# Kernel tuning notes

Measured on AMD Instinct MI355X. Metric: run time of the kernel, lower is better.

## Reference

```python
import jax, jax.numpy as jnp
import numpy as np

GS = 14           # group_size = (14, 14); N must equal GS*GS
NUM_HEADS = 4
DIM = 128
POS_DIM = (DIM // 4) // 4  # 8
EPS = 1e-5


def _ln(x, g, b):
    mu = x.mean(-1, keepdims=True)
    var = ((x - mu) ** 2).mean(-1, keepdims=True)
    return (x - mu) * jax.lax.rsqrt(var + EPS) * g + b


def setup_inputs() -> dict:
    key = jax.random.key(0)
    ks = jax.random.split(key, 20)
    B, N, C = 1024, GS * GS, DIM
    s = lambda fan: 1.0 / np.sqrt(fan)
    inp = {
        "x": jax.random.normal(ks[0], (B, N, C), jnp.float32),
        # linear weights stored as [in, out] (torch W.T)
        "wq": jax.random.normal(ks[1], (C, C), jnp.float32) * s(C),
        "wkv": jax.random.normal(ks[2], (C, 2 * C), jnp.float32) * s(C),
        "wproj": jax.random.normal(ks[3], (C, C), jnp.float32) * s(C),
        "bproj": jnp.zeros((C,), jnp.float32),
        "pp_w": jax.random.normal(ks[4], (2, POS_DIM), jnp.float32) * s(2),
        "pp_b": jnp.zeros((POS_DIM,), jnp.float32),
        "ln1_g": jnp.ones((POS_DIM,), jnp.float32),
        "ln1_b": jnp.zeros((POS_DIM,), jnp.float32),
        "l1_w": jax.random.normal(ks[5], (POS_DIM, POS_DIM), jnp.float32) * s(POS_DIM),
        "l1_b": jnp.zeros((POS_DIM,), jnp.float32),
        "ln2_g": jnp.ones((POS_DIM,), jnp.float32),
        "ln2_b": jnp.zeros((POS_DIM,), jnp.float32),
        "l2_w": jax.random.normal(ks[6], (POS_DIM, POS_DIM), jnp.float32) * s(POS_DIM),
        "l2_b": jnp.zeros((POS_DIM,), jnp.float32),
        "ln3_g": jnp.ones((POS_DIM,), jnp.float32),
        "ln3_b": jnp.zeros((POS_DIM,), jnp.float32),
        "l3_w": jax.random.normal(ks[7], (POS_DIM, NUM_HEADS), jnp.float32) * s(POS_DIM),
        "l3_b": jnp.zeros((NUM_HEADS,), jnp.float32),
    }
    return inp


def _rel_pos_index():
    # relative_position_index for square window (len(group_size)==2 branch)
    ch = jnp.arange(GS)
    coords = jnp.stack(jnp.meshgrid(ch, ch, indexing="ij"))        # [2, GS, GS]
    cf = coords.reshape(2, -1)                                       # [2, N]
    rel = cf[:, :, None] - cf[:, None, :]                            # [2, N, N]
    rel = rel.transpose(1, 2, 0)                                     # [N, N, 2]
    rel = rel + jnp.array([GS - 1, GS - 1])
    idx = rel[..., 0] * (2 * GS - 1) + rel[..., 1]                   # [N, N]
    return idx


def _biases():
    p = jnp.arange(1 - GS, GS)
    b = jnp.stack(jnp.meshgrid(p, p, indexing="ij"))                 # [2, 2GS-1, 2GS-1]
    return b.reshape(2, -1).T.astype(jnp.float32)                    # [(2GS-1)^2, 2]


def reference(x, wq, wkv, wproj, bproj, pp_w, pp_b,
              ln1_g, ln1_b, l1_w, l1_b,
              ln2_g, ln2_b, l2_w, l2_b,
              ln3_g, ln3_b, l3_w, l3_b):
    B, N, C = x.shape
    H = NUM_HEADS
    hd = C // H
    scale = hd ** -0.5

    q = (x @ wq).reshape(B, N, H, hd).transpose(0, 2, 1, 3)          # [B,H,N,hd]
    kv = (x @ wkv).reshape(B, N, 2, H, hd)
    k = kv[:, :, 0].transpose(0, 2, 1, 3)                            # [B,H,N,hd]
    v = kv[:, :, 1].transpose(0, 2, 1, 3)

    attn = jnp.einsum("bhqd,bhkd->bhqk", q, k) * scale               # [B,H,N,N]

    # dynamic position bias: tiny MLP over relative coords, residual=False path
    pos = _biases() @ pp_w + pp_b                                    # [M, pos_dim]
    pos = jax.nn.relu(_ln(pos, ln1_g, ln1_b)) @ l1_w + l1_b
    pos = jax.nn.relu(_ln(pos, ln2_g, ln2_b)) @ l2_w + l2_b
    pos = jax.nn.relu(_ln(pos, ln3_g, ln3_b)) @ l3_w + l3_b          # [M, H]

    rpb = pos[_rel_pos_index()]                                      # [N,N,H] gather
    attn = attn + rpb.transpose(2, 0, 1)[None]                       # [B,H,N,N]

    attn = jax.nn.softmax(attn, axis=-1)
    out = jnp.einsum("bhqk,bhkd->bhqd", attn, v)                     # [B,H,N,hd]
    out = out.transpose(0, 2, 1, 3).reshape(B, N, C)
    return out @ wproj + bproj
```

## Files before the change

kernel.cpp:

```cpp
#include <hip/hip_runtime.h>

typedef __attribute__((ext_vector_type(8))) __bf16 bf16x8;
typedef __attribute__((ext_vector_type(4))) __bf16 bf16x4;
typedef __attribute__((ext_vector_type(4))) float f32x4;
typedef __attribute__((ext_vector_type(4))) short s16x4;

#define MFMA32(a,b,c) __builtin_amdgcn_mfma_f32_16x16x32_bf16(a, b, c, 0, 0, 0)

static __device__ inline f32x4 MFMAX16(s16x4 a, s16x4 b, f32x4 c) {
#if __has_builtin(__builtin_amdgcn_mfma_f32_16x16x16bf16_1k)
  return __builtin_amdgcn_mfma_f32_16x16x16bf16_1k(a, b, c, 0, 0, 0);
#else
  f32x4 d;
  asm("v_mfma_f32_16x16x16_bf16 %0, %1, %2, %3" : "=v"(d) : "v"(a), "v"(b), "v"(c));
  return d;
#endif
}

#define KS 36
#define VS 212
#define NW 4

__device__ inline bf16x8 load_a_f32(const float* p) {
  const float4* q = (const float4*)p;
  float4 u = q[0], v = q[1];
  bf16x8 r;
  r[0] = (__bf16)u.x; r[1] = (__bf16)u.y; r[2] = (__bf16)u.z; r[3] = (__bf16)u.w;
  r[4] = (__bf16)v.x; r[5] = (__bf16)v.y; r[6] = (__bf16)v.z; r[7] = (__bf16)v.w;
  return r;
}

__device__ inline void lnrelu8(float* v, const float* g, const float* bta) {
  float mu = 0.f;
#pragma unroll
  for (int i = 0; i < 8; i++) mu += v[i];
  mu *= 0.125f;
  float var = 0.f;
#pragma unroll
  for (int i = 0; i < 8; i++) { float d = v[i] - mu; var += d * d; }
  var *= 0.125f;
  float inv = rsqrtf(var + 1e-5f);
#pragma unroll
  for (int i = 0; i < 8; i++) v[i] = fmaxf((v[i] - mu) * inv * g[i] + bta[i], 0.f);
}

__global__ void k_prep(const float* __restrict__ wq, const float* __restrict__ wkv,
                       const float* __restrict__ wproj,
                       const float* __restrict__ pp_w, const float* __restrict__ pp_b,
                       const float* ln1_g, const float* ln1_b, const float* l1_w, const float* l1_b,
                       const float* ln2_g, const float* ln2_b, const float* l2_w, const float* l2_b,
                       const float* ln3_g, const float* ln3_b, const float* l3_w, const float* l3_b,
                       __bf16* __restrict__ wF, __bf16* __restrict__ wpT,
                       __bf16* __restrict__ biasT) {
  __shared__ float pos_s[4 * 729];
  int blk = blockIdx.x, tid = threadIdx.x;
  if (blk < 88) {
    int t = blk * 256 + tid;
    if (t < 6144) {
      int lane = t & 63, frag = t >> 6;
      int kc = frag & 3, nt = (frag >> 2) & 1, tt = (frag >> 3) % 3, h = frag / 24;
      int col = lane & 15, quad = lane >> 4;
      int o = h * 32 + nt * 16 + col;
      int ibase = kc * 32 + quad * 8;
      bf16x8 vv;
#pragma unroll
      for (int j = 0; j < 8; j++) {
        int in = ibase + j;
        float w = (tt == 0) ? wq[in * 128 + o]
                : (tt == 1) ? wkv[in * 256 + o]
                            : wkv[in * 256 + 128 + o];
        vv[j] = (__bf16)w;
      }
      *(bf16x8*)&wF[(size_t)t * 8] = vv;
    } else if (t < 6144 + 16384) {
      int t2 = t - 6144;
      int o = t2 >> 7, i = t2 & 127;
      wpT[t2] = (__bf16)wproj[i * 128 + o];
    }
    return;
  }
  for (int m = tid; m < 729; m += 256) {
    float dr = (float)(m / 27) - 13.f, dc = (float)(m % 27) - 13.f;
    float a[8], bv[8];
#pragma unroll
    for (int j = 0; j < 8; j++) a[j] = dr * pp_w[j] + dc * pp_w[8 + j] + pp_b[j];
    lnrelu8(a, ln1_g, ln1_b);
#pragma unroll
    for (int o = 0; o < 8; o++) {
      float s = l1_b[o];
#pragma unroll
      for (int j = 0; j < 8; j++) s += a[j] * l1_w[j * 8 + o];
      bv[o] = s;
    }
    lnrelu8(bv, ln2_g, ln2_b);
#pragma unroll
    for (int o = 0; o < 8; o++) {
      float s = l2_b[o];
#pragma unroll
      for (int j = 0; j < 8; j++) s += bv[j] * l2_w[j * 8 + o];
      a[o] = s;
    }
    lnrelu8(a, ln3_g, ln3_b);
#pragma unroll
    for (int o = 0; o < 4; o++) {
      float s = l3_b[o];
#pragma unroll
      for (int j = 0; j < 8; j++) s += a[j] * l3_w[j * 4 + o];
      pos_s[o * 729 + m] = s;
    }
  }
  __syncthreads();
  int t = (blk - 88) * 256 + tid;
  int g = t % 52; int rem = t / 52; int qi = rem % 208; int h = rem / 208;
  int kj0 = g * 4;
  int r1 = qi / 14, c1 = qi % 14;
  bf16x4 o;
#pragma unroll
  for (int r = 0; r < 4; r++) {
    int kj = kj0 + r;
    float v = 0.f;
    if (qi < 196 && kj < 196) {
      int r2 = kj / 14, c2 = kj % 14;
      v = pos_s[h * 729 + (r1 - r2 + 13) * 27 + (c1 - c2 + 13)];
    }
    o[r] = (__bf16)v;
  }
  *(bf16x4*)&biasT[((size_t)(h * 208 + qi)) * 208 + kj0] = o;
}

__launch_bounds__(256, 4)
__global__ void k_attn(const float* __restrict__ x, const __bf16* __restrict__ wF,
                       const __bf16* __restrict__ biasT, __bf16* __restrict__ Og) {
  __shared__ __align__(16) __bf16 k_s[208 * KS];
  __shared__ __align__(16) __bf16 vT_s[32 * VS];

  int tid = threadIdx.x;
  int wv = tid >> 6, lane = tid & 63, col = lane & 15, quad = lane >> 4;
  int bi = blockIdx.x;
  int b = (bi & 7) * 128 + (bi >> 5);
  int h = (bi >> 3) & 3;

  const __bf16* wH = wF + (size_t)h * 12288;
#define WG(t, nt, kc) (*(const bf16x8*)&wH[(((t) * 2 + (nt)) * 4 + (kc)) * 512 + lane * 8])

  const float* xb = x + (size_t)b * (196 * 128);
  const float scale = 0.17677669529663687f;

  s16x4 qb[4][2];

#pragma unroll
  for (int i = 0; i < 4; i++) {
    int qt = wv + i * NW;
    if (qt < 13) {
      int row = qt * 16 + col;
      const float* ap = xb + (size_t)(row < 196 ? row : 0) * 128 + quad * 8;
      bf16x8 xf[4];
#pragma unroll
      for (int kc = 0; kc < 4; kc++) xf[kc] = load_a_f32(ap + kc * 32);
#pragma unroll
      for (int nt = 0; nt < 2; nt++) {
        f32x4 acc = {0.f, 0.f, 0.f, 0.f};
#pragma unroll
        for (int kc = 0; kc < 4; kc++) acc = MFMA32(WG(1, nt, kc), xf[kc], acc);
        bf16x4 pk;
#pragma unroll
        for (int r = 0; r < 4; r++) pk[r] = (__bf16)acc[r];
        *(bf16x4*)&k_s[row * KS + nt * 16 + quad * 4] = pk;
      }
#pragma unroll
      for (int nt = 0; nt < 2; nt++) {
        f32x4 acc = {0.f, 0.f, 0.f, 0.f};
#pragma unroll
        for (int kc = 0; kc < 4; kc++) acc = MFMA32(xf[kc], WG(2, nt, kc), acc);
        bf16x4 pk;
#pragma unroll
        for (int r = 0; r < 4; r++) pk[r] = (__bf16)acc[r];
        *(bf16x4*)&vT_s[(nt * 16 + col) * VS + qt * 16 + quad * 4] = pk;
      }
#pragma unroll
      for (int nt = 0; nt < 2; nt++) {
        f32x4 acc = {0.f, 0.f, 0.f, 0.f};
#pragma unroll
        for (int kc = 0; kc < 4; kc++) acc = MFMA32(WG(0, nt, kc), xf[kc], acc);
        bf16x4 pk;
#pragma unroll
        for (int r = 0; r < 4; r++) pk[r] = (__bf16)(acc[r] * scale);
        qb[i][nt] = __builtin_bit_cast(s16x4, pk);
      }
    }
  }
  __syncthreads();

#pragma unroll
  for (int i = 0; i < 4; i++) {
    int qt = wv + i * NW;
    if (qt < 13) {
      int qi = qt * 16 + col;
      const __bf16* brow = biasT + ((size_t)(h * 208 + qi)) * 208 + quad * 4;
      bf16x4 bl[13];
#pragma unroll
      for (int kt = 0; kt < 13; kt++) bl[kt] = *(const bf16x4*)(brow + kt * 16);

      float sum = 0.f;
      s16x4 pp[13];
#pragma unroll
      for (int kt = 0; kt < 13; kt++) {
        s16x4 ka0 = *(const s16x4*)&k_s[(kt * 16 + col) * KS + quad * 4];
        s16x4 ka1 = *(const s16x4*)&k_s[(kt * 16 + col) * KS + 16 + quad * 4];
        f32x4 acc = {0.f, 0.f, 0.f, 0.f};
        acc = MFMAX16(ka0, qb[i][0], acc);
        acc = MFMAX16(ka1, qb[i][1], acc);
        bf16x4 pk;
#pragma unroll
        for (int r = 0; r < 4; r++) {
          float e = __expf(acc[r] + (float)bl[kt][r]);
          if (kt == 12 && quad != 0) e = 0.f;
          sum += e;
          pk[r] = (__bf16)e;
        }
        pp[kt] = __builtin_bit_cast(s16x4, pk);
      }
      sum += __shfl_xor(sum, 16);
      sum += __shfl_xor(sum, 32);
      float inv = 1.f / sum;

      f32x4 o0a = {0.f,0.f,0.f,0.f}, o0b = {0.f,0.f,0.f,0.f};
      f32x4 o1a = {0.f,0.f,0.f,0.f}, o1b = {0.f,0.f,0.f,0.f};
#pragma unroll
      for (int kt = 0; kt < 13; kt++) {
        s16x4 va0 = *(const s16x4*)&vT_s[col * VS + kt * 16 + quad * 4];
        s16x4 va1 = *(const s16x4*)&vT_s[(16 + col) * VS + kt * 16 + quad * 4];
        if (kt & 1) { o0b = MFMAX16(va0, pp[kt], o0b); o1b = MFMAX16(va1, pp[kt], o1b); }
        else        { o0a = MFMAX16(va0, pp[kt], o0a); o1a = MFMAX16(va1, pp[kt], o1a); }
      }
      if (qi < 196) {
        __bf16* og = Og + ((size_t)b * 196 + qi) * 128 + h * 32;
        bf16x4 s0, s1;
#pragma unroll
        for (int r = 0; r < 4; r++) {
          s0[r] = (__bf16)((o0a[r] + o0b[r]) * inv);
          s1[r] = (__bf16)((o1a[r] + o1b[r]) * inv);
        }
        *(bf16x4*)&og[quad * 4]      = s0;
        *(bf16x4*)&og[16 + quad * 4] = s1;
      }
    }
  }
#undef WG
}

__launch_bounds__(256, 4)
__global__ void k_proj(const __bf16* __restrict__ Og, const __bf16* __restrict__ wpT,
                       const float* __restrict__ bproj, float* __restrict__ out) {
  int tid = threadIdx.x, wv = tid >> 6, lane = tid & 63, col = lane & 15, quad = lane >> 4;
  size_t rb = (size_t)blockIdx.x * 64 + wv * 16;
  const __bf16* arow = Og + (rb + col) * 128 + quad * 8;
  bf16x8 af[4];
#pragma unroll
  for (int kc = 0; kc < 4; kc++) af[kc] = *(const bf16x8*)(arow + kc * 32);
#pragma unroll
  for (int nt = 0; nt < 8; nt++) {
    f32x4 acc = {0.f, 0.f, 0.f, 0.f};
#pragma unroll
    for (int kc = 0; kc < 4; kc++)
      acc = MFMA32(*(const bf16x8*)&wpT[(size_t)(nt * 16 + col) * 128 + kc * 32 + quad * 8],
                   af[kc], acc);
    int od = nt * 16 + quad * 4;
    float4 bp = *(const float4*)&bproj[od];
    float4 st = { acc[0] + bp.x, acc[1] + bp.y, acc[2] + bp.z, acc[3] + bp.w };
    *(float4*)&out[(rb + col) * 128 + od] = st;
  }
}

extern "C" void kernel_launch(void* const* d_in, const int* in_sizes, int n_in,
                              void* d_out, int out_size, void* d_ws, size_t ws_size,
                              hipStream_t stream) {
  const float* x     = (const float*)d_in[0];
  const float* wq    = (const float*)d_in[1];
  const float* wkv   = (const float*)d_in[2];
  const float* wproj = (const float*)d_in[3];
  const float* bproj = (const float*)d_in[4];
  const float* pp_w  = (const float*)d_in[5];
  const float* pp_b  = (const float*)d_in[6];
  const float* ln1_g = (const float*)d_in[7];
  const float* ln1_b = (const float*)d_in[8];
  const float* l1_w  = (const float*)d_in[9];
  const float* l1_b  = (const float*)d_in[10];
  const float* ln2_g = (const float*)d_in[11];
  const float* ln2_b = (const float*)d_in[12];
  const float* l2_w  = (const float*)d_in[13];
  const float* l2_b  = (const float*)d_in[14];
  const float* ln3_g = (const float*)d_in[15];
  const float* ln3_b = (const float*)d_in[16];
  const float* l3_w  = (const float*)d_in[17];
  const float* l3_b  = (const float*)d_in[18];
  float* out = (float*)d_out;

  char* ws = (char*)d_ws;
  __bf16* wF    = (__bf16*)ws;
  __bf16* wpT   = (__bf16*)(ws + 98304);
  __bf16* biasT = (__bf16*)(ws + 131072);
  __bf16* Og    = (__bf16*)(ws + 477184);

  k_prep<<<257, 256, 0, stream>>>(wq, wkv, wproj, pp_w, pp_b,
                                  ln1_g, ln1_b, l1_w, l1_b,
                                  ln2_g, ln2_b, l2_w, l2_b,
                                  ln3_g, ln3_b, l3_w, l3_b,
                                  wF, wpT, biasT);
  k_attn<<<4096, 256, 0, stream>>>(x, wF, biasT, Og);
  k_proj<<<3136, 256, 0, stream>>>(Og, wpT, bproj, out);
}
```

Baseline: 383.8 us.

## Prefetch x and bias tiles, fuse softmax with PV, use exp2

The x rows for the next q-tile and the next bias tile are now loaded into registers while the current tile is computed, so global load latency overlaps with MFMA work. The bias is stored in a per-lane contiguous layout and pre-scaled by log2e, with the scale folded into q, so the exponent becomes a native exp2. The K tile in LDS is interleaved (KS 40) so each lane reads both K halves in one 16-byte load. The P·V accumulation is fused into the score loop, which removes the pp[13] staging array. Register pressure rises from holding the prefetched x and bias values, which could hurt occupancy under launch_bounds(256,4).

```diff
diff --git a/kernel.cpp b/kernel.cpp
--- a/kernel.cpp
+++ b/kernel.cpp
@@ -4,6 +4,7 @@
 typedef __attribute__((ext_vector_type(4))) __bf16 bf16x4;
 typedef __attribute__((ext_vector_type(4))) float f32x4;
 typedef __attribute__((ext_vector_type(4))) short s16x4;
+typedef __attribute__((ext_vector_type(8))) short s16x8;
 
 #define MFMA32(a,b,c) __builtin_amdgcn_mfma_f32_16x16x32_bf16(a, b, c, 0, 0, 0)
 
@@ -17,18 +18,10 @@
 #endif
 }
 
-#define KS 36
+#define KS 40
 #define VS 212
 #define NW 4
-
-__device__ inline bf16x8 load_a_f32(const float* p) {
-  const float4* q = (const float4*)p;
-  float4 u = q[0], v = q[1];
-  bf16x8 r;
-  r[0] = (__bf16)u.x; r[1] = (__bf16)u.y; r[2] = (__bf16)u.z; r[3] = (__bf16)u.w;
-  r[4] = (__bf16)v.x; r[5] = (__bf16)v.y; r[6] = (__bf16)v.z; r[7] = (__bf16)v.w;
-  return r;
-}
+#define LOG2E 1.4426950408889634f
 
 __device__ inline void lnrelu8(float* v, const float* g, const float* bta) {
   float mu = 0.f;
@@ -51,7 +44,7 @@
                        const float* ln2_g, const float* ln2_b, const float* l2_w, const float* l2_b,
                        const float* ln3_g, const float* ln3_b, const float* l3_w, const float* l3_b,
                        __bf16* __restrict__ wF, __bf16* __restrict__ wpT,
-                       __bf16* __restrict__ biasT) {
+                       __bf16* __restrict__ biasP) {
   __shared__ float pos_s[4 * 729];
   int blk = blockIdx.x, tid = threadIdx.x;
   if (blk < 88) {
@@ -112,6 +105,7 @@
   __syncthreads();
   int t = (blk - 88) * 256 + tid;
   int g = t % 52; int rem = t / 52; int qi = rem % 208; int h = rem / 208;
+  int kt = g >> 2, qd = g & 3;
   int kj0 = g * 4;
   int r1 = qi / 14, c1 = qi % 14;
   bf16x4 o;
@@ -123,14 +117,14 @@
       int r2 = kj / 14, c2 = kj % 14;
       v = pos_s[h * 729 + (r1 - r2 + 13) * 27 + (c1 - c2 + 13)];
     }
-    o[r] = (__bf16)v;
-  }
-  *(bf16x4*)&biasT[((size_t)(h * 208 + qi)) * 208 + kj0] = o;
+    o[r] = (__bf16)(v * LOG2E);
+  }
+  *(bf16x4*)&biasP[(((size_t)h * 208 + qi) * 4 + qd) * 52 + kt * 4] = o;
 }
 
 __launch_bounds__(256, 4)
 __global__ void k_attn(const float* __restrict__ x, const __bf16* __restrict__ wF,
-                       const __bf16* __restrict__ biasT, __bf16* __restrict__ Og) {
+                       const __bf16* __restrict__ biasP, __bf16* __restrict__ Og) {
   __shared__ __align__(16) __bf16 k_s[208 * KS];
   __shared__ __align__(16) __bf16 vT_s[32 * VS];
 
@@ -144,19 +138,39 @@
 #define WG(t, nt, kc) (*(const bf16x8*)&wH[(((t) * 2 + (nt)) * 4 + (kc)) * 512 + lane * 8])
 
   const float* xb = x + (size_t)b * (196 * 128);
-  const float scale = 0.17677669529663687f;
+  const float scale = 0.17677669529663687f * LOG2E;
 
   s16x4 qb[4][2];
+  float4 xr[8];
+
+  {
+    int row0 = wv * 16 + col;
+    const float4* q4 = (const float4*)(xb + (size_t)(row0 < 196 ? row0 : 0) * 128 + quad * 8);
+#pragma unroll
+    for (int kc = 0; kc < 4; kc++) { xr[2 * kc] = q4[kc * 8]; xr[2 * kc + 1] = q4[kc * 8 + 1]; }
+  }
 
 #pragma unroll
   for (int i = 0; i < 4; i++) {
     int qt = wv + i * NW;
     if (qt < 13) {
+      bf16x8 xf[4];
+#pragma unroll
+      for (int kc = 0; kc < 4; kc++) {
+        float4 u = xr[2 * kc], v = xr[2 * kc + 1];
+        bf16x8 r;
+        r[0] = (__bf16)u.x; r[1] = (__bf16)u.y; r[2] = (__bf16)u.z; r[3] = (__bf16)u.w;
+        r[4] = (__bf16)v.x; r[5] = (__bf16)v.y; r[6] = (__bf16)v.z; r[7] = (__bf16)v.w;
+        xf[kc] = r;
+      }
+      int qn = qt + NW;
+      if (i < 3 && qn < 13) {
+        int row = qn * 16 + col;
+        const float4* q4 = (const float4*)(xb + (size_t)(row < 196 ? row : 0) * 128 + quad * 8);
+#pragma unroll
+        for (int kc = 0; kc < 4; kc++) { xr[2 * kc] = q4[kc * 8]; xr[2 * kc + 1] = q4[kc * 8 + 1]; }
+      }
       int row = qt * 16 + col;
-      const float* ap = xb + (size_t)(row < 196 ? row : 0) * 128 + quad * 8;
-      bf16x8 xf[4];
-#pragma unroll
-      for (int kc = 0; kc < 4; kc++) xf[kc] = load_a_f32(ap + kc * 32);
 #pragma unroll
       for (int nt = 0; nt < 2; nt++) {
         f32x4 acc = {0.f, 0.f, 0.f, 0.f};
@@ -165,7 +179,7 @@
         bf16x4 pk;
 #pragma unroll
         for (int r = 0; r < 4; r++) pk[r] = (__bf16)acc[r];
-        *(bf16x4*)&k_s[row * KS + nt * 16 + quad * 4] = pk;
+        *(bf16x4*)&k_s[row * KS + quad * 8 + nt * 4] = pk;
       }
 #pragma unroll
       for (int nt = 0; nt < 2; nt++) {
@@ -188,6 +202,14 @@
         qb[i][nt] = __builtin_bit_cast(s16x4, pk);
       }
     }
+  }
+
+  bf16x4 bl[13];
+  {
+    int qi0 = wv * 16 + col;
+    const __bf16* bp = biasP + (((size_t)h * 208 + qi0) * 4 + quad) * 52;
+#pragma unroll
+    for (int kt = 0; kt < 13; kt++) bl[kt] = *(const bf16x4*)(bp + kt * 4);
   }
   __syncthreads();
 
@@ -196,43 +218,40 @@
     int qt = wv + i * NW;
     if (qt < 13) {
       int qi = qt * 16 + col;
-      const __bf16* brow = biasT + ((size_t)(h * 208 + qi)) * 208 + quad * 4;
-      bf16x4 bl[13];
-#pragma unroll
-      for (int kt = 0; kt < 13; kt++) bl[kt] = *(const bf16x4*)(brow + kt * 16);
+      int qn = qt + NW;
+      bool nxt = (i < 3) && (qn < 13);
+      const __bf16* bpn = biasP + (((size_t)h * 208 + (qn * 16 + col)) * 4 + quad) * 52;
 
       float sum = 0.f;
-      s16x4 pp[13];
+      f32x4 o0a = {0.f,0.f,0.f,0.f}, o0b = {0.f,0.f,0.f,0.f};
+      f32x4 o1a = {0.f,0.f,0.f,0.f}, o1b = {0.f,0.f,0.f,0.f};
 #pragma unroll
       for (int kt = 0; kt < 13; kt++) {
-        s16x4 ka0 = *(const s16x4*)&k_s[(kt * 16 + col) * KS + quad * 4];
-        s16x4 ka1 = *(const s16x4*)&k_s[(kt * 16 + col) * KS + 16 + quad * 4];
+        s16x8 ka = *(const s16x8*)&k_s[(kt * 16 + col) * KS + quad * 8];
+        s16x4 ka0 = __builtin_shufflevector(ka, ka, 0, 1, 2, 3);
+        s16x4 ka1 = __builtin_shufflevector(ka, ka, 4, 5, 6, 7);
         f32x4 acc = {0.f, 0.f, 0.f, 0.f};
         acc = MFMAX16(ka0, qb[i][0], acc);
         acc = MFMAX16(ka1, qb[i][1], acc);
+        bf16x4 b4 = bl[kt];
+        if (nxt) bl[kt] = *(const bf16x4*)(bpn + kt * 4);
         bf16x4 pk;
 #pragma unroll
         for (int r = 0; r < 4; r++) {
-          float e = __expf(acc[r] + (float)bl[kt][r]);
+          float e = __builtin_amdgcn_exp2f(acc[r] + (float)b4[r]);
           if (kt == 12 && quad != 0) e = 0.f;
           sum += e;
           pk[r] = (__bf16)e;
         }
-        pp[kt] = __builtin_bit_cast(s16x4, pk);
+        s16x4 pv = __builtin_bit_cast(s16x4, pk);
+        s16x4 va0 = *(const s16x4*)&vT_s[col * VS + kt * 16 + quad * 4];
+        s16x4 va1 = *(const s16x4*)&vT_s[(16 + col) * VS + kt * 16 + quad * 4];
+        if (kt & 1) { o0b = MFMAX16(va0, pv, o0b); o1b = MFMAX16(va1, pv, o1b); }
+        else        { o0a = MFMAX16(va0, pv, o0a); o1a = MFMAX16(va1, pv, o1a); }
       }
       sum += __shfl_xor(sum, 16);
       sum += __shfl_xor(sum, 32);
       float inv = 1.f / sum;
-
-      f32x4 o0a = {0.f,0.f,0.f,0.f}, o0b = {0.f,0.f,0.f,0.f};
-      f32x4 o1a = {0.f,0.f,0.f,0.f}, o1b = {0.f,0.f,0.f,0.f};
-#pragma unroll
-      for (int kt = 0; kt < 13; kt++) {
-        s16x4 va0 = *(const s16x4*)&vT_s[col * VS + kt * 16 + quad * 4];
-        s16x4 va1 = *(const s16x4*)&vT_s[(16 + col) * VS + kt * 16 + quad * 4];
-        if (kt & 1) { o0b = MFMAX16(va0, pp[kt], o0b); o1b = MFMAX16(va1, pp[kt], o1b); }
-        else        { o0a = MFMAX16(va0, pp[kt], o0a); o1a = MFMAX16(va1, pp[kt], o1a); }
-      }
       if (qi < 196) {
         __bf16* og = Og + ((size_t)b * 196 + qi) * 128 + h * 32;
         bf16x4 s0, s1;
@@ -299,14 +318,14 @@
   char* ws = (char*)d_ws;
   __bf16* wF    = (__bf16*)ws;
   __bf16* wpT   = (__bf16*)(ws + 98304);
-  __bf16* biasT = (__bf16*)(ws + 131072);
+  __bf16* biasP = (__bf16*)(ws + 131072);
   __bf16* Og    = (__bf16*)(ws + 477184);
 
   k_prep<<<257, 256, 0, stream>>>(wq, wkv, wproj, pp_w, pp_b,
                                   ln1_g, ln1_b, l1_w, l1_b,
                                   ln2_g, ln2_b, l2_w, l2_b,
                                   ln3_g, ln3_b, l3_w, l3_b,
-                                  wF, wpT, biasT);
-  k_attn<<<4096, 256, 0, stream>>>(x, wF, biasT, Og);
+                                  wF, wpT, biasP);
+  k_attn<<<4096, 256, 0, stream>>>(x, wF, biasP, Og);
   k_proj<<<3136, 256, 0, stream>>>(Og, wpT, bproj, out);
 }
```

After: 415.5 us. 8.2% more time.
